# Optimization experiments

Hardware: AMD Instinct MI355X
Metric: run time of the kernel (lower is better)

Reference implementation:

```python
import jax, jax.numpy as jnp
import numpy as np

B, T, D, H = 4, 1024, 1024, 16


def setup_inputs() -> dict:
    key = jax.random.key(0)
    ks = jax.random.split(key, 6)
    s = 0.02  # small init so softmax is well-conditioned
    return {
        "x": jax.random.normal(ks[0], (B, T, D), jnp.float32),
        "position_embedding": jax.random.normal(ks[1], (B, T, D), jnp.float32),
        "Wc": jax.random.normal(ks[2], (2 * D, D), jnp.float32) * s,
        "bc": jnp.zeros((2 * D,), jnp.float32),
        "Wp": jax.random.normal(ks[3], (D, D), jnp.float32) * s,
        "bp": jnp.zeros((D,), jnp.float32),
        "Wo": jax.random.normal(ks[4], (D, D), jnp.float32) * s,
        "bo": jnp.zeros((D,), jnp.float32),
        "num_heads": H,
    }


def reference(x, position_embedding, Wc, bc, Wp, bp, Wo, bo, num_heads):
    b, t, d = x.shape
    h = num_heads
    hd = d // h
    scale = hd ** -0.5
    # content projection -> q, k  (value reuses content k, as in the original)
    cqk = (x @ Wc.T + bc).reshape(b, t, 2, h, hd)
    q = cqk[:, :, 0]  # [B,T,H,hd]
    k = cqk[:, :, 1]  # [B,T,H,hd]
    # position keys
    pk = (position_embedding @ Wp.T + bp).reshape(b, t, h, hd)
    # dual-stream scores: content-content + content-position
    scores = (jnp.einsum('bqhd,bkhd->bhqk', q, k)
              + jnp.einsum('bqhd,bkhd->bhqk', q, pk)) * scale
    attn = jax.nn.softmax(scores, axis=-1)  # dropout is identity in eval
    out = jnp.einsum('bhqk,bkhd->bqhd', attn, k).reshape(b, t, d)
    return out @ Wo.T + bo, attn
```

## Files before the change

kernel.cpp:

```cpp
#include <hip/hip_runtime.h>
#include <hip/hip_bf16.h>

#define BB 4
#define TT 1024
#define DD 1024
#define HH 16
#define HDIM 64
#define MM (BB*TT)

typedef unsigned short u16;
typedef __attribute__((ext_vector_type(8))) short bf16x8;
typedef __attribute__((ext_vector_type(8))) _Float16 f16x8;
typedef __attribute__((ext_vector_type(4))) float f32x4;
typedef __attribute__((ext_vector_type(4))) unsigned short u16x4;

__device__ __forceinline__ u16 f2bf(float f) {
    union { float f; unsigned u; } v; v.f = f;
    return (u16)((v.u + 0x7fffu + ((v.u >> 16) & 1u)) >> 16);
}
__device__ __forceinline__ float bf2f(u16 h) {
    union { unsigned u; float f; } v; v.u = ((unsigned)h) << 16; return v.f;
}
__device__ __forceinline__ u16 f2h(float f) {
    union { _Float16 h; u16 u; } v; v.h = (_Float16)f;
    return v.u;
}

__device__ __forceinline__ void gload16(const void* g, void* l) {
    __builtin_amdgcn_global_load_lds(
        (const __attribute__((address_space(1))) unsigned int*)g,
        (__attribute__((address_space(3))) unsigned int*)l, 16, 0, 0);
}

template<bool TO_FP16>
__global__ __launch_bounds__(256)
void cvt_kernel(const float* __restrict__ src, u16* __restrict__ dst)
{
    const size_t i = ((size_t)blockIdx.x * 256 + threadIdx.x) * 4;
    const float4 v = *(const float4*)&src[i];
    u16x4 o;
    if constexpr (TO_FP16) {
        o[0] = f2h(v.x); o[1] = f2h(v.y); o[2] = f2h(v.z); o[3] = f2h(v.w);
    } else {
        o[0] = f2bf(v.x); o[1] = f2bf(v.y); o[2] = f2bf(v.z); o[3] = f2bf(v.w);
    }
    *(u16x4*)&dst[i] = o;
}

__global__ __launch_bounds__(256)
void ktrans_kernel(const u16* __restrict__ k16, u16* __restrict__ k16T)
{
    __shared__ u16 tmp[64][72];
    const int tc = blockIdx.x, h = blockIdx.y, b = blockIdx.z;
    const size_t hb = ((size_t)(b * HH + h)) << 16;
    const int tid = threadIdx.x;
    const int sr = tid >> 2, sc = (tid & 3) * 8;
    *(bf16x8*)&tmp[sr][sc]      = *(const bf16x8*)&k16[hb + (size_t)(tc * 64 + sr) * HDIM + sc];
    *(bf16x8*)&tmp[sr][sc + 32] = *(const bf16x8*)&k16[hb + (size_t)(tc * 64 + sr) * HDIM + sc + 32];
    __syncthreads();
#pragma unroll
    for (int half = 0; half < 2; ++half) {
        bf16x8 v;
#pragma unroll
        for (int j = 0; j < 8; ++j) v[j] = (short)tmp[sc + half * 32 + j][sr];
        *(bf16x8*)&k16T[hb + (size_t)sr * TT + tc * 64 + sc + half * 32] = v;
    }
}

template<bool FP16, int MODE>
__global__ __launch_bounds__(256)
void gemm_mfma(const u16* __restrict__ Ah, const u16* __restrict__ Bh,
               const float* __restrict__ bias,
               float* __restrict__ dstF, u16* __restrict__ dstH1,
               u16* __restrict__ dstH2, const float* __restrict__ kaux,
               const int M, const int N, const int K)
{
    __shared__ u16 As[128][64];
    __shared__ u16 Bs[128][64];

    const int tid  = threadIdx.x;
    const int w    = tid >> 6;
    const int lane = tid & 63;
    const int lg   = lane >> 4;
    const int lr   = lane & 15;
    const int wr   = w >> 1, wc = w & 1;
    const int m0   = blockIdx.y * 128, n0 = blockIdx.x * 128;

    const f32x4 zero = {0.f, 0.f, 0.f, 0.f};
    f32x4 acc[4][4];
#pragma unroll
    for (int i = 0; i < 4; ++i)
#pragma unroll
        for (int j = 0; j < 4; ++j) acc[i][j] = zero;

    const int srow = tid >> 3;
    const int scol = (tid & 7) * 8;
    const int ldr  = w << 3;

    for (int k0 = 0; k0 < K; k0 += 64) {
        __syncthreads();
#pragma unroll
        for (int i = 0; i < 4; ++i) {
            const size_t ga = (size_t)(m0 + i * 32 + srow) * K + k0 + scol;
            const size_t gb = (size_t)(n0 + i * 32 + srow) * K + k0 + scol;
            gload16(&Ah[ga], &As[i * 32 + ldr][0]);
            gload16(&Bh[gb], &Bs[i * 32 + ldr][0]);
        }
        __syncthreads();
#pragma unroll
        for (int kk = 0; kk < 2; ++kk) {
            const int koff = kk * 32 + lg * 8;
#pragma unroll
            for (int mf = 0; mf < 4; ++mf) {
#pragma unroll
                for (int nf = 0; nf < 4; ++nf) {
                    if constexpr (FP16) {
                        const f16x8 a = *(const f16x8*)&As[wr * 64 + mf * 16 + lr][koff];
                        const f16x8 b = *(const f16x8*)&Bs[wc * 64 + nf * 16 + lr][koff];
                        acc[mf][nf] = __builtin_amdgcn_mfma_f32_16x16x32_f16(a, b, acc[mf][nf], 0, 0, 0);
                    } else {
                        const bf16x8 a = *(const bf16x8*)&As[wr * 64 + mf * 16 + lr][koff];
                        const bf16x8 b = *(const bf16x8*)&Bs[wc * 64 + nf * 16 + lr][koff];
                        acc[mf][nf] = __builtin_amdgcn_mfma_f32_16x16x32_bf16(a, b, acc[mf][nf], 0, 0, 0);
                    }
                }
            }
        }
    }

#pragma unroll
    for (int mf = 0; mf < 4; ++mf)
#pragma unroll
        for (int nf = 0; nf < 4; ++nf)
#pragma unroll
            for (int j = 0; j < 4; ++j) {
                const int gm = m0 + wr * 64 + mf * 16 + lg * 4 + j;
                const int gn = n0 + wc * 64 + nf * 16 + lr;
                const float v = acc[mf][nf][j] + bias[gn];
                if constexpr (MODE == 0) {
                    const int bb = gm >> 10, t = gm & 1023;
                    const int c = gn >> 10, hh = (gn & 1023) >> 6, d = gn & 63;
                    const size_t idx = ((((size_t)bb * HH + hh) << 10) + t) * HDIM + d;
                    if (c == 0) dstH1[idx] = f2bf(v * 0.125f);
                    else { dstF[idx] = v; dstH2[idx] = f2bf(v); }
                } else if constexpr (MODE == 1) {
                    const int bb = gm >> 10, t = gm & 1023;
                    const int hh = gn >> 6, d = gn & 63;
                    const size_t idx = ((((size_t)bb * HH + hh) << 10) + t) * HDIM + d;
                    dstH1[idx] = f2bf(v + kaux[idx]);
                } else {
                    dstF[(size_t)gm * N + gn] = v;
                }
            }
}

__global__ __launch_bounds__(256)
void attn_mfma(const u16* __restrict__ qg, const u16* __restrict__ kTg,
               const u16* __restrict__ kpg,
               float* __restrict__ attn, u16* __restrict__ ch)
{
    __shared__ u16 kp_s[64][72];
    __shared__ u16 kT_s[64][72];
    __shared__ u16 P_s[4][16][72];

    const int tid  = threadIdx.x;
    const int w    = tid >> 6;
    const int lane = tid & 63;
    const int lg   = lane >> 4;
    const int lr   = lane & 15;
    const int q0   = blockIdx.x * 64;
    const int h = blockIdx.y, b = blockIdx.z;
    const size_t hb = ((size_t)(b * HH + h)) << 16;

    bf16x8 qf0, qf1;
    {
        const size_t base = hb + (size_t)(q0 + w * 16 + lr) * HDIM + lg * 8;
        qf0 = *(const bf16x8*)&qg[base];
        qf1 = *(const bf16x8*)&qg[base + 32];
    }

    const int sr = tid >> 2;
    const int sc = (tid & 3) * 8;

    float rs[4] = {0.f, 0.f, 0.f, 0.f};
    for (int t = 0; t < TT / 64; ++t) {
        const size_t kvbase = hb + (size_t)(t * 64) * HDIM;
        __syncthreads();
        *(bf16x8*)&kp_s[sr][sc]      = *(const bf16x8*)&kpg[kvbase + sr * HDIM + sc];
        *(bf16x8*)&kp_s[sr][sc + 32] = *(const bf16x8*)&kpg[kvbase + sr * HDIM + sc + 32];
        __syncthreads();
#pragma unroll
        for (int ct = 0; ct < 4; ++ct) {
            f32x4 acc = {0.f, 0.f, 0.f, 0.f};
            const bf16x8 b0 = *(const bf16x8*)&kp_s[ct * 16 + lr][lg * 8];
            const bf16x8 b1 = *(const bf16x8*)&kp_s[ct * 16 + lr][lg * 8 + 32];
            acc = __builtin_amdgcn_mfma_f32_16x16x32_bf16(qf0, b0, acc, 0, 0, 0);
            acc = __builtin_amdgcn_mfma_f32_16x16x32_bf16(qf1, b1, acc, 0, 0, 0);
#pragma unroll
            for (int j = 0; j < 4; ++j) rs[j] += __expf(acc[j]);
        }
    }
#pragma unroll
    for (int off = 1; off < 16; off <<= 1) {
#pragma unroll
        for (int j = 0; j < 4; ++j) rs[j] += __shfl_xor(rs[j], off);
    }
    float ri[4];
#pragma unroll
    for (int j = 0; j < 4; ++j) ri[j] = 1.f / rs[j];

    f32x4 cacc[4] = {{0,0,0,0},{0,0,0,0},{0,0,0,0},{0,0,0,0}};
    const size_t abase = ((((size_t)b * HH + h) << 10) + q0 + w * 16) << 10;

    for (int t = 0; t < TT / 64; ++t) {
        const size_t kvbase = hb + (size_t)(t * 64) * HDIM;
        __syncthreads();
        *(bf16x8*)&kp_s[sr][sc]      = *(const bf16x8*)&kpg[kvbase + sr * HDIM + sc];
        *(bf16x8*)&kp_s[sr][sc + 32] = *(const bf16x8*)&kpg[kvbase + sr * HDIM + sc + 32];
        *(bf16x8*)&kT_s[sr][sc]      = *(const bf16x8*)&kTg[hb + (size_t)sr * TT + t * 64 + sc];
        *(bf16x8*)&kT_s[sr][sc + 32] = *(const bf16x8*)&kTg[hb + (size_t)sr * TT + t * 64 + sc + 32];
        __syncthreads();
#pragma unroll
        for (int ct = 0; ct < 4; ++ct) {
            f32x4 acc = {0.f, 0.f, 0.f, 0.f};
            const bf16x8 b0 = *(const bf16x8*)&kp_s[ct * 16 + lr][lg * 8];
            const bf16x8 b1 = *(const bf16x8*)&kp_s[ct * 16 + lr][lg * 8 + 32];
            acc = __builtin_amdgcn_mfma_f32_16x16x32_bf16(qf0, b0, acc, 0, 0, 0);
            acc = __builtin_amdgcn_mfma_f32_16x16x32_bf16(qf1, b1, acc, 0, 0, 0);
            const int col = t * 64 + ct * 16 + lr;
#pragma unroll
            for (int j = 0; j < 4; ++j) {
                const float p = __expf(acc[j]) * ri[j];
                attn[abase + (size_t)(lg * 4 + j) * TT + col] = p;
                P_s[w][lg * 4 + j][ct * 16 + lr] = f2bf(p);
            }
        }
        asm volatile("s_waitcnt lgkmcnt(0)" ::: "memory");
        const bf16x8 pa0 = *(const bf16x8*)&P_s[w][lr][lg * 8];
        const bf16x8 pa1 = *(const bf16x8*)&P_s[w][lr][lg * 8 + 32];
#pragma unroll
        for (int dt = 0; dt < 4; ++dt) {
            const bf16x8 kb0 = *(const bf16x8*)&kT_s[dt * 16 + lr][lg * 8];
            const bf16x8 kb1 = *(const bf16x8*)&kT_s[dt * 16 + lr][lg * 8 + 32];
            cacc[dt] = __builtin_amdgcn_mfma_f32_16x16x32_bf16(pa0, kb0, cacc[dt], 0, 0, 0);
            cacc[dt] = __builtin_amdgcn_mfma_f32_16x16x32_bf16(pa1, kb1, cacc[dt], 0, 0, 0);
        }
    }

#pragma unroll
    for (int dt = 0; dt < 4; ++dt)
#pragma unroll
        for (int j = 0; j < 4; ++j) {
            const int qr = q0 + w * 16 + lg * 4 + j;
            ch[(((size_t)b << 10) + qr) * DD + h * HDIM + dt * 16 + lr] = f2bf(cacc[dt][j]);
        }
}

extern "C" void kernel_launch(void* const* d_in, const int* in_sizes, int n_in,
                              void* d_out, int out_size, void* d_ws, size_t ws_size,
                              hipStream_t stream)
{
    const float* x  = (const float*)d_in[0];
    const float* pe = (const float*)d_in[1];
    const float* Wc = (const float*)d_in[2];
    const float* bc = (const float*)d_in[3];
    const float* Wp = (const float*)d_in[4];
    const float* bp = (const float*)d_in[5];
    const float* Wo = (const float*)d_in[6];
    const float* bo = (const float*)d_in[7];

    float* out  = (float*)d_out;
    float* attn = out + (size_t)MM * DD;

    char* ws = (char*)d_ws;
    float* kf32 = (float*)(ws);
    u16* q16  = (u16*)(ws + ((size_t)16 << 20));
    u16* k16  = (u16*)(ws + ((size_t)24 << 20));
    u16* kp16 = (u16*)(ws + ((size_t)32 << 20));
    u16* x16  = (u16*)(ws + ((size_t)40 << 20));
    u16* Wc16 = (u16*)(ws + ((size_t)56 << 20));
    u16* k16T = (u16*)(ws + ((size_t)56 << 20));
    u16* pe16 = x16;
    u16* Wp16 = (u16*)(ws + ((size_t)24 << 20));
    u16* chh  = x16;
    u16* Wo16 = (u16*)(ws + ((size_t)48 << 20));

    cvt_kernel<true><<<4096, 256, 0, stream>>>(x, x16);
    cvt_kernel<true><<<2048, 256, 0, stream>>>(Wc, Wc16);
    gemm_mfma<true, 0><<<dim3(16, 32), 256, 0, stream>>>(
        x16, Wc16, bc, kf32, q16, k16, nullptr, MM, 2048, DD);
    ktrans_kernel<<<dim3(16, HH, BB), 256, 0, stream>>>(k16, k16T);
    cvt_kernel<true><<<4096, 256, 0, stream>>>(pe, pe16);
    cvt_kernel<true><<<1024, 256, 0, stream>>>(Wp, Wp16);
    gemm_mfma<true, 1><<<dim3(8, 32), 256, 0, stream>>>(
        pe16, Wp16, bp, nullptr, kp16, nullptr, kf32, MM, 1024, DD);
    attn_mfma<<<dim3(TT / 64, HH, BB), 256, 0, stream>>>(
        q16, k16T, kp16, attn, chh);
    cvt_kernel<false><<<1024, 256, 0, stream>>>(Wo, Wo16);
    gemm_mfma<false, 2><<<dim3(8, 32), 256, 0, stream>>>(
        chh, Wo16, bo, out, nullptr, nullptr, nullptr, MM, 1024, DD);
}
```

Measured before the change: 209.4 us.

## Double-buffer K tiles in attention kernel with register prefetch

Both passes of the attention kernel now keep two LDS buffers for the key tiles. The next tile's global loads go into registers before the current tile's MFMA work and are written to the alternate buffer afterward. This overlaps global memory latency with compute and removes one barrier per iteration. In exchange it doubles LDS use for the K tiles and raises register pressure, which may lower occupancy.

Measured after the change: 202.8 us. 3.1% less time.

```diff
diff --git a/kernel.cpp b/kernel.cpp
--- a/kernel.cpp
+++ b/kernel.cpp
@@ -159,8 +159,8 @@
                const u16* __restrict__ kpg,
                float* __restrict__ attn, u16* __restrict__ ch)
 {
-    __shared__ u16 kp_s[64][72];
-    __shared__ u16 kT_s[64][72];
+    __shared__ u16 kp_s[2][64][72];
+    __shared__ u16 kT_s[2][64][72];
     __shared__ u16 P_s[4][16][72];
 
     const int tid  = threadIdx.x;
@@ -181,25 +181,43 @@
 
     const int sr = tid >> 2;
     const int sc = (tid & 3) * 8;
+    bf16x8 ra, rb, rc, rd;
+
+    ra = *(const bf16x8*)&kpg[hb + (size_t)sr * HDIM + sc];
+    rb = *(const bf16x8*)&kpg[hb + (size_t)sr * HDIM + sc + 32];
+    *(bf16x8*)&kp_s[0][sr][sc]      = ra;
+    *(bf16x8*)&kp_s[0][sr][sc + 32] = rb;
+    __syncthreads();
 
     float rs[4] = {0.f, 0.f, 0.f, 0.f};
     for (int t = 0; t < TT / 64; ++t) {
-        const size_t kvbase = hb + (size_t)(t * 64) * HDIM;
-        __syncthreads();
-        *(bf16x8*)&kp_s[sr][sc]      = *(const bf16x8*)&kpg[kvbase + sr * HDIM + sc];
-        *(bf16x8*)&kp_s[sr][sc + 32] = *(const bf16x8*)&kpg[kvbase + sr * HDIM + sc + 32];
-        __syncthreads();
+        const int cur = t & 1;
+        if (t < 15) {
+            const size_t nb = hb + (size_t)((t + 1) * 64 + sr) * HDIM;
+            ra = *(const bf16x8*)&kpg[nb + sc];
+            rb = *(const bf16x8*)&kpg[nb + sc + 32];
+        }
 #pragma unroll
         for (int ct = 0; ct < 4; ++ct) {
             f32x4 acc = {0.f, 0.f, 0.f, 0.f};
-            const bf16x8 b0 = *(const bf16x8*)&kp_s[ct * 16 + lr][lg * 8];
-            const bf16x8 b1 = *(const bf16x8*)&kp_s[ct * 16 + lr][lg * 8 + 32];
+            const bf16x8 b0 = *(const bf16x8*)&kp_s[cur][ct * 16 + lr][lg * 8];
+            const bf16x8 b1 = *(const bf16x8*)&kp_s[cur][ct * 16 + lr][lg * 8 + 32];
             acc = __builtin_amdgcn_mfma_f32_16x16x32_bf16(qf0, b0, acc, 0, 0, 0);
             acc = __builtin_amdgcn_mfma_f32_16x16x32_bf16(qf1, b1, acc, 0, 0, 0);
 #pragma unroll
             for (int j = 0; j < 4; ++j) rs[j] += __expf(acc[j]);
         }
-    }
+        if (t < 15) {
+            *(bf16x8*)&kp_s[cur ^ 1][sr][sc]      = ra;
+            *(bf16x8*)&kp_s[cur ^ 1][sr][sc + 32] = rb;
+        }
+        __syncthreads();
+    }
+
+    ra = *(const bf16x8*)&kpg[hb + (size_t)sr * HDIM + sc];
+    rb = *(const bf16x8*)&kpg[hb + (size_t)sr * HDIM + sc + 32];
+    rc = *(const bf16x8*)&kTg[hb + (size_t)sr * TT + sc];
+    rd = *(const bf16x8*)&kTg[hb + (size_t)sr * TT + sc + 32];
 #pragma unroll
     for (int off = 1; off < 16; off <<= 1) {
 #pragma unroll
@@ -208,23 +226,30 @@
     float ri[4];
 #pragma unroll
     for (int j = 0; j < 4; ++j) ri[j] = 1.f / rs[j];
+    *(bf16x8*)&kp_s[0][sr][sc]      = ra;
+    *(bf16x8*)&kp_s[0][sr][sc + 32] = rb;
+    *(bf16x8*)&kT_s[0][sr][sc]      = rc;
+    *(bf16x8*)&kT_s[0][sr][sc + 32] = rd;
+    __syncthreads();
 
     f32x4 cacc[4] = {{0,0,0,0},{0,0,0,0},{0,0,0,0},{0,0,0,0}};
     const size_t abase = ((((size_t)b * HH + h) << 10) + q0 + w * 16) << 10;
 
     for (int t = 0; t < TT / 64; ++t) {
-        const size_t kvbase = hb + (size_t)(t * 64) * HDIM;
-        __syncthreads();
-        *(bf16x8*)&kp_s[sr][sc]      = *(const bf16x8*)&kpg[kvbase + sr * HDIM + sc];
-        *(bf16x8*)&kp_s[sr][sc + 32] = *(const bf16x8*)&kpg[kvbase + sr * HDIM + sc + 32];
-        *(bf16x8*)&kT_s[sr][sc]      = *(const bf16x8*)&kTg[hb + (size_t)sr * TT + t * 64 + sc];
-        *(bf16x8*)&kT_s[sr][sc + 32] = *(const bf16x8*)&kTg[hb + (size_t)sr * TT + t * 64 + sc + 32];
-        __syncthreads();
+        const int cur = t & 1;
+        if (t < 15) {
+            const size_t nb = hb + (size_t)((t + 1) * 64 + sr) * HDIM;
+            ra = *(const bf16x8*)&kpg[nb + sc];
+            rb = *(const bf16x8*)&kpg[nb + sc + 32];
+            const size_t tb = hb + (size_t)sr * TT + (t + 1) * 64;
+            rc = *(const bf16x8*)&kTg[tb + sc];
+            rd = *(const bf16x8*)&kTg[tb + sc + 32];
+        }
 #pragma unroll
         for (int ct = 0; ct < 4; ++ct) {
             f32x4 acc = {0.f, 0.f, 0.f, 0.f};
-            const bf16x8 b0 = *(const bf16x8*)&kp_s[ct * 16 + lr][lg * 8];
-            const bf16x8 b1 = *(const bf16x8*)&kp_s[ct * 16 + lr][lg * 8 + 32];
+            const bf16x8 b0 = *(const bf16x8*)&kp_s[cur][ct * 16 + lr][lg * 8];
+            const bf16x8 b1 = *(const bf16x8*)&kp_s[cur][ct * 16 + lr][lg * 8 + 32];
             acc = __builtin_amdgcn_mfma_f32_16x16x32_bf16(qf0, b0, acc, 0, 0, 0);
             acc = __builtin_amdgcn_mfma_f32_16x16x32_bf16(qf1, b1, acc, 0, 0, 0);
             const int col = t * 64 + ct * 16 + lr;
@@ -240,11 +265,18 @@
         const bf16x8 pa1 = *(const bf16x8*)&P_s[w][lr][lg * 8 + 32];
 #pragma unroll
         for (int dt = 0; dt < 4; ++dt) {
-            const bf16x8 kb0 = *(const bf16x8*)&kT_s[dt * 16 + lr][lg * 8];
-            const bf16x8 kb1 = *(const bf16x8*)&kT_s[dt * 16 + lr][lg * 8 + 32];
+            const bf16x8 kb0 = *(const bf16x8*)&kT_s[cur][dt * 16 + lr][lg * 8];
+            const bf16x8 kb1 = *(const bf16x8*)&kT_s[cur][dt * 16 + lr][lg * 8 + 32];
             cacc[dt] = __builtin_amdgcn_mfma_f32_16x16x32_bf16(pa0, kb0, cacc[dt], 0, 0, 0);
             cacc[dt] = __builtin_amdgcn_mfma_f32_16x16x32_bf16(pa1, kb1, cacc[dt], 0, 0, 0);
         }
+        if (t < 15) {
+            *(bf16x8*)&kp_s[cur ^ 1][sr][sc]      = ra;
+            *(bf16x8*)&kp_s[cur ^ 1][sr][sc + 32] = rb;
+            *(bf16x8*)&kT_s[cur ^ 1][sr][sc]      = rc;
+            *(bf16x8*)&kT_s[cur ^ 1][sr][sc + 32] = rd;
+        }
+        __syncthreads();
     }
 
 #pragma unroll
```
